# Kernel tuning notes

Hardware: AMD Instinct MI355X
Metric: run time of the kernel (lower is better)

## Reference

```python
import jax, jax.numpy as jnp
import numpy as np

N_MAX = 20
REG_WEIGHT = 0.01


def setup_inputs() -> dict:
    key = jax.random.key(0)
    k1, k2, k3, k4 = jax.random.split(key, 4)
    target = jax.random.normal(k1, (32, 512, 2048), dtype=jnp.float32)
    pred = jax.random.normal(k2, (32, 512, 2048), dtype=jnp.float32)
    latent = jax.random.normal(k3, (64800,), dtype=jnp.float32)
    # R_xyz: xyz coordinates of each field point (buffer from get_field()), shape [3, G]
    R_xyz = jax.random.normal(k4, (3, 64800), dtype=jnp.float32)
    return {"target": target, "pred": pred, "latent": latent, "R_xyz": R_xyz}


def reference(target, pred, latent, R_xyz):
    # L1 loss (mean reduction)
    l1 = jnp.mean(jnp.abs(target - pred))

    # Regularizer: std of pairwise distances of the xyz positions of the
    # top-N_max latent activations.
    _, idx = jax.lax.top_k(latent, N_MAX)          # [N_max] int indices
    max_xyz = R_xyz[:, idx].T                       # [N_max, 3]

    # F.pdist(p=2): upper-triangle (i<j) pairwise Euclidean distances
    iu, ju = jnp.triu_indices(N_MAX, k=1)
    diff = max_xyz[iu] - max_xyz[ju]                # [N_max*(N_max-1)/2, 3]
    dists = jnp.sqrt(jnp.sum(diff * diff, axis=-1))

    # torch.std defaults to unbiased (ddof=1)
    reg = jnp.std(dists, ddof=1)

    total = l1 + REG_WEIGHT * reg
    return (total, l1, REG_WEIGHT * reg)
```

## Files before the change

kernel.cpp:

```cpp
#include <hip/hip_runtime.h>
#include <hip/hip_bf16.h>

#define NMAX 20
#define NPAIR (NMAX * (NMAX - 1) / 2)
#define TPB 256
#define L1_BLOCKS 2048
#define TOPK_BLOCKS 16

__device__ __forceinline__ unsigned long long packKey(float v, unsigned i) {
    unsigned u = __float_as_uint(v);
    u = (u & 0x80000000u) ? ~u : (u | 0x80000000u);
    return ((unsigned long long)u << 32) | (unsigned long long)(~i);
}

__global__ void __launch_bounds__(TPB)
fused_kernel(const float4* __restrict__ t, const float4* __restrict__ p, int nvec,
             const float* __restrict__ latent, int nLat,
             float* __restrict__ partial, unsigned long long* __restrict__ keysOut) {
    if (blockIdx.x >= TOPK_BLOCKS) {
        int bid = blockIdx.x - TOPK_BLOCKS;
        float s = 0.f;
        int stride = L1_BLOCKS * TPB;
        for (int i = bid * TPB + threadIdx.x; i < nvec; i += stride) {
            float4 a = t[i];
            float4 b = p[i];
            s += fabsf(a.x - b.x) + fabsf(a.y - b.y) +
                 fabsf(a.z - b.z) + fabsf(a.w - b.w);
        }
        #pragma unroll
        for (int o = 32; o > 0; o >>= 1) s += __shfl_down(s, o, 64);
        __shared__ float wsum[TPB / 64];
        int lane = threadIdx.x & 63;
        int wid  = threadIdx.x >> 6;
        if (lane == 0) wsum[wid] = s;
        __syncthreads();
        if (threadIdx.x == 0) {
            float tot = 0.f;
            #pragma unroll
            for (int w = 0; w < TPB / 64; ++w) tot += wsum[w];
            partial[bid] = tot;
        }
    } else {
        int b   = blockIdx.x;
        int tid = threadIdx.x;
        int lane = tid & 63, wid = tid >> 6;

        unsigned long long loc[NMAX];
        #pragma unroll
        for (int k = 0; k < NMAX; ++k) loc[k] = 0ull;

        for (int i = b * TPB + tid; i < nLat; i += TOPK_BLOCKS * TPB) {
            unsigned long long key = packKey(latent[i], (unsigned)i);
            #pragma unroll
            for (int k = NMAX - 1; k >= 1; --k) {
                loc[k] = (key > loc[k - 1]) ? loc[k - 1]
                                            : ((key > loc[k]) ? key : loc[k]);
            }
            loc[0] = (key > loc[0]) ? key : loc[0];
        }

        __shared__ unsigned long long wmax[TPB / 64];
        __shared__ unsigned long long selk;
        unsigned long long prev = ~0ull;
        for (int r = 0; r < NMAX; ++r) {
            unsigned long long m = 0ull;
            #pragma unroll
            for (int k = 0; k < NMAX; ++k) {
                unsigned long long c = loc[k];
                m = (c < prev && c > m) ? c : m;
            }
            #pragma unroll
            for (int o = 32; o > 0; o >>= 1) {
                unsigned long long other = __shfl_down(m, o, 64);
                if (other > m) m = other;
            }
            if (lane == 0) wmax[wid] = m;
            __syncthreads();
            if (tid == 0) {
                unsigned long long mm = wmax[0];
                #pragma unroll
                for (int w = 1; w < TPB / 64; ++w) if (wmax[w] > mm) mm = wmax[w];
                selk = mm;
                keysOut[b * NMAX + r] = mm;
            }
            __syncthreads();
            prev = selk;
        }
    }
}

__global__ void __launch_bounds__(TPB)
finalize_kernel(const float* __restrict__ partials, int nPartials,
                const unsigned long long* __restrict__ keys,
                const float* __restrict__ R_xyz, int G,
                float* __restrict__ out, float invN) {
    __shared__ float red[TPB];
    __shared__ unsigned long long ck[TOPK_BLOCKS * NMAX];
    __shared__ unsigned long long wmax[TPB / 64];
    __shared__ unsigned long long selk;
    __shared__ int   sel[NMAX];
    __shared__ float sxyz[NMAX][3];
    __shared__ float s_l1, s_sum;

    int tid = threadIdx.x, lane = tid & 63, wid = tid >> 6;

    {
        float s = 0.f;
        for (int i = tid; i < nPartials; i += TPB) s += partials[i];
        red[tid] = s;
        __syncthreads();
        for (int off = TPB / 2; off > 0; off >>= 1) {
            if (tid < off) red[tid] += red[tid + off];
            __syncthreads();
        }
        if (tid == 0) s_l1 = red[0] * invN;
        __syncthreads();
    }

    for (int i = tid; i < TOPK_BLOCKS * NMAX; i += TPB) ck[i] = keys[i];
    __syncthreads();
    {
        unsigned long long prev = ~0ull;
        for (int r = 0; r < NMAX; ++r) {
            unsigned long long m = 0ull;
            for (int i = tid; i < TOPK_BLOCKS * NMAX; i += TPB) {
                unsigned long long c = ck[i];
                m = (c < prev && c > m) ? c : m;
            }
            #pragma unroll
            for (int o = 32; o > 0; o >>= 1) {
                unsigned long long other = __shfl_down(m, o, 64);
                if (other > m) m = other;
            }
            if (lane == 0) wmax[wid] = m;
            __syncthreads();
            if (tid == 0) {
                unsigned long long mm = wmax[0];
                #pragma unroll
                for (int w = 1; w < TPB / 64; ++w) if (wmax[w] > mm) mm = wmax[w];
                selk = mm;
                sel[r] = (int)(~(unsigned)mm);
            }
            __syncthreads();
            prev = selk;
        }
    }

    if (tid < NMAX * 3) {
        int i = tid / 3, d = tid % 3;
        sxyz[i][d] = R_xyz[d * G + sel[i]];
    }
    __syncthreads();

    float dval = 0.f;
    if (tid < NPAIR) {
        int k = tid, i = 0, rem = NMAX - 1;
        while (k >= rem) { k -= rem; ++i; --rem; }
        int j = i + 1 + k;
        float dx = sxyz[i][0] - sxyz[j][0];
        float dy = sxyz[i][1] - sxyz[j][1];
        float dz = sxyz[i][2] - sxyz[j][2];
        dval = sqrtf(dx * dx + dy * dy + dz * dz);
    }
    red[tid] = dval;
    __syncthreads();
    for (int off = TPB / 2; off > 0; off >>= 1) {
        if (tid < off) red[tid] += red[tid + off];
        __syncthreads();
    }
    if (tid == 0) s_sum = red[0];
    __syncthreads();
    red[tid] = dval * dval;
    __syncthreads();
    for (int off = TPB / 2; off > 0; off >>= 1) {
        if (tid < off) red[tid] += red[tid + off];
        __syncthreads();
    }
    if (tid == 0) {
        float sum   = s_sum;
        float sumsq = red[0];
        float mean  = sum / (float)NPAIR;
        float var   = (sumsq - (float)NPAIR * mean * mean) / (float)(NPAIR - 1);
        float stdv  = sqrtf(fmaxf(var, 0.f));
        float reg   = 0.01f * stdv;
        out[0] = s_l1 + reg;
        out[1] = s_l1;
        out[2] = reg;
    }
}

extern "C" void kernel_launch(void* const* d_in, const int* in_sizes, int n_in,
                              void* d_out, int out_size, void* d_ws, size_t ws_size,
                              hipStream_t stream) {
    const float* target = (const float*)d_in[0];
    const float* pred   = (const float*)d_in[1];
    const float* latent = (const float*)d_in[2];
    const float* R_xyz  = (const float*)d_in[3];
    float* out = (float*)d_out;

    int n    = in_sizes[0];
    int nLat = in_sizes[2];
    int G    = in_sizes[3] / 3;
    int nvec = n / 4;

    float* partials = (float*)d_ws;
    unsigned long long* keys = (unsigned long long*)((char*)d_ws + L1_BLOCKS * sizeof(float));

    fused_kernel<<<TOPK_BLOCKS + L1_BLOCKS, TPB, 0, stream>>>(
        (const float4*)target, (const float4*)pred, nvec,
        latent, nLat, partials, keys);

    finalize_kernel<<<1, TPB, 0, stream>>>(
        partials, L1_BLOCKS, keys, R_xyz, G, out, 1.0f / (float)n);
}
```

Before: 72.69 us.

## Double-buffer L1 streaming via global_load_lds and fold top-k into L1 blocks

Rewrites the L1 reduction to stream chunks of target and pred straight into LDS with async global_load_lds, double-buffered so the next chunk's loads overlap compute on the current one. The grid is halved to 1024 blocks, and the first 16 blocks run the top-k scan after their L1 work instead of using dedicated blocks. This aims to raise memory-level parallelism and cut block scheduling overhead. In exchange it adds LDS pressure and makes top-k serialized behind the L1 work in those blocks. There is also no explicit wait on the async loads beyond __syncthreads, so correctness depends on how the compiler handles vmcnt.

Result: slower. 84.16 us (+15.8%).

```diff
diff --git a/kernel.cpp b/kernel.cpp
--- a/kernel.cpp
+++ b/kernel.cpp
@@ -4,8 +4,15 @@
 #define NMAX 20
 #define NPAIR (NMAX * (NMAX - 1) / 2)
 #define TPB 256
-#define L1_BLOCKS 2048
 #define TOPK_BLOCKS 16
+#define L1_BLOCKS 1024
+#define CHUNK 512
+
+typedef float f4 __attribute__((ext_vector_type(4)));
+
+#define GLD16(gp, lp) __builtin_amdgcn_global_load_lds(                        \
+    (__attribute__((address_space(1))) void*)(gp),                             \
+    (__attribute__((address_space(3))) void*)(lp), 16, 0, 0)
 
 __device__ __forceinline__ unsigned long long packKey(float v, unsigned i) {
     unsigned u = __float_as_uint(v);
@@ -13,38 +20,69 @@
     return ((unsigned long long)u << 32) | (unsigned long long)(~i);
 }
 
-__global__ void __launch_bounds__(TPB)
-fused_kernel(const float4* __restrict__ t, const float4* __restrict__ p, int nvec,
-             const float* __restrict__ latent, int nLat,
-             float* __restrict__ partial, unsigned long long* __restrict__ keysOut) {
-    if (blockIdx.x >= TOPK_BLOCKS) {
-        int bid = blockIdx.x - TOPK_BLOCKS;
-        float s = 0.f;
-        int stride = L1_BLOCKS * TPB;
-        for (int i = bid * TPB + threadIdx.x; i < nvec; i += stride) {
-            float4 a = t[i];
-            float4 b = p[i];
-            s += fabsf(a.x - b.x) + fabsf(a.y - b.y) +
-                 fabsf(a.z - b.z) + fabsf(a.w - b.w);
-        }
+__device__ __forceinline__ float absdiff4(f4 a, f4 b) {
+    return fabsf(a.x - b.x) + fabsf(a.y - b.y) +
+           fabsf(a.z - b.z) + fabsf(a.w - b.w);
+}
+
+__global__ void __launch_bounds__(TPB, 4)
+l1_topk_kernel(const f4* __restrict__ t, const f4* __restrict__ p, int nvec,
+               const float* __restrict__ latent, int nLat,
+               float* __restrict__ partial, unsigned long long* __restrict__ keysOut,
+               int rounds) {
+    __shared__ f4 lA[2][CHUNK];
+    __shared__ f4 lB[2][CHUNK];
+    __shared__ float red[TPB / 64];
+    __shared__ unsigned long long wmax[TPB / 64];
+    __shared__ unsigned long long selk;
+
+    int tid = threadIdx.x, lane = tid & 63, w = tid >> 6;
+    int b = blockIdx.x;
+
+    float acc = 0.f;
+
+    {
+        long base = (long)b * CHUNK + w * 128 + lane;
+        GLD16(t + base,      &lA[0][w * 128]);
+        GLD16(t + base + 64, &lA[0][w * 128 + 64]);
+        GLD16(p + base,      &lB[0][w * 128]);
+        GLD16(p + base + 64, &lB[0][w * 128 + 64]);
+    }
+
+    for (int r = 0; r < rounds; ++r) {
+        int d = r & 1;
+        __syncthreads();
+        acc += absdiff4(lA[d][tid],       lB[d][tid]);
+        acc += absdiff4(lA[d][tid + 256], lB[d][tid + 256]);
+
+        if (r + 1 < rounds) {
+            long c = (long)(r + 1) * L1_BLOCKS + b;
+            long base = c * CHUNK + w * 128 + lane;
+            GLD16(t + base,      &lA[d ^ 1][w * 128]);
+            GLD16(t + base + 64, &lA[d ^ 1][w * 128 + 64]);
+            GLD16(p + base,      &lB[d ^ 1][w * 128]);
+            GLD16(p + base + 64, &lB[d ^ 1][w * 128 + 64]);
+        }
+    }
+
+    {
+        long done = (long)rounds * L1_BLOCKS * CHUNK;
+        for (long i = done + (long)b * TPB + tid; i < nvec; i += (long)L1_BLOCKS * TPB)
+            acc += absdiff4(t[i], p[i]);
+    }
+
+    #pragma unroll
+    for (int o = 32; o > 0; o >>= 1) acc += __shfl_down(acc, o, 64);
+    if (lane == 0) red[w] = acc;
+    __syncthreads();
+    if (tid == 0) {
+        float tot = 0.f;
         #pragma unroll
-        for (int o = 32; o > 0; o >>= 1) s += __shfl_down(s, o, 64);
-        __shared__ float wsum[TPB / 64];
-        int lane = threadIdx.x & 63;
-        int wid  = threadIdx.x >> 6;
-        if (lane == 0) wsum[wid] = s;
-        __syncthreads();
-        if (threadIdx.x == 0) {
-            float tot = 0.f;
-            #pragma unroll
-            for (int w = 0; w < TPB / 64; ++w) tot += wsum[w];
-            partial[bid] = tot;
-        }
-    } else {
-        int b   = blockIdx.x;
-        int tid = threadIdx.x;
-        int lane = tid & 63, wid = tid >> 6;
-
+        for (int k = 0; k < TPB / 64; ++k) tot += red[k];
+        partial[b] = tot;
+    }
+
+    if (b < TOPK_BLOCKS) {
         unsigned long long loc[NMAX];
         #pragma unroll
         for (int k = 0; k < NMAX; ++k) loc[k] = 0ull;
@@ -59,8 +97,6 @@
             loc[0] = (key > loc[0]) ? key : loc[0];
         }
 
-        __shared__ unsigned long long wmax[TPB / 64];
-        __shared__ unsigned long long selk;
         unsigned long long prev = ~0ull;
         for (int r = 0; r < NMAX; ++r) {
             unsigned long long m = 0ull;
@@ -74,12 +110,12 @@
                 unsigned long long other = __shfl_down(m, o, 64);
                 if (other > m) m = other;
             }
-            if (lane == 0) wmax[wid] = m;
+            if (lane == 0) wmax[w] = m;
             __syncthreads();
             if (tid == 0) {
                 unsigned long long mm = wmax[0];
                 #pragma unroll
-                for (int w = 1; w < TPB / 64; ++w) if (wmax[w] > mm) mm = wmax[w];
+                for (int k = 1; k < TPB / 64; ++k) if (wmax[k] > mm) mm = wmax[k];
                 selk = mm;
                 keysOut[b * NMAX + r] = mm;
             }
@@ -202,13 +238,14 @@
     int nLat = in_sizes[2];
     int G    = in_sizes[3] / 3;
     int nvec = n / 4;
+    int rounds = nvec / (L1_BLOCKS * CHUNK);
 
     float* partials = (float*)d_ws;
     unsigned long long* keys = (unsigned long long*)((char*)d_ws + L1_BLOCKS * sizeof(float));
 
-    fused_kernel<<<TOPK_BLOCKS + L1_BLOCKS, TPB, 0, stream>>>(
-        (const float4*)target, (const float4*)pred, nvec,
-        latent, nLat, partials, keys);
+    l1_topk_kernel<<<L1_BLOCKS, TPB, 0, stream>>>(
+        (const f4*)target, (const f4*)pred, nvec,
+        latent, nLat, partials, keys, rounds);
 
     finalize_kernel<<<1, TPB, 0, stream>>>(
         partials, L1_BLOCKS, keys, R_xyz, G, out, 1.0f / (float)n);
```
